# Performance work log

Hardware: AMD Instinct MI355X
Metric: run time of the kernel (lower is better)

## Reference

```python
import jax, jax.numpy as jnp
import numpy as np

B, C, H, W = 4, 512, 64, 64  # batch, channels (query_dim=model_dim), spatial

def _conv1x1(x, Wm, bias):
    # 1x1 conv == channel-mixing matmul: (b,c,h,w),(o,c) -> (b,o,h,w)
    return jnp.einsum('bchw,oc->bohw', x, Wm) + bias[None, :, None, None]

def setup_inputs() -> dict:
    key = jax.random.key(0)
    ks = jax.random.split(key, 9)
    s = 0.02
    return {
        'q':  jax.random.normal(ks[0], (B, C, H, W), dtype=jnp.float32),
        'Wq': jax.random.normal(ks[1], (C, C), dtype=jnp.float32) * s,
        'bq': jax.random.normal(ks[2], (C,), dtype=jnp.float32) * s,
        'Wk': jax.random.normal(ks[3], (C, C), dtype=jnp.float32) * s,
        'bk': jax.random.normal(ks[4], (C,), dtype=jnp.float32) * s,
        'Wv': jax.random.normal(ks[5], (C, C), dtype=jnp.float32) * s,
        'bv': jax.random.normal(ks[6], (C,), dtype=jnp.float32) * s,
        'Wo': jax.random.normal(ks[7], (C, C), dtype=jnp.float32) * s,
        'bo': jax.random.normal(ks[8], (C,), dtype=jnp.float32) * s,
    }

def reference(q, Wq, bq, Wk, bk, Wv, bv, Wo, bo):
    b, c, h, w = q.shape
    # separate=True, k=v=q (get_qkv defaults)
    qp = _conv1x1(q, Wq, bq)
    kp = _conv1x1(q, Wk, bk)
    vp = _conv1x1(q, Wv, bv)
    # view_in: b c h w -> b (h w) c  (single head; heads are NOT split)
    def flat(x):
        return x.reshape(b, c, h * w).transpose(0, 2, 1)  # (b, s, c)
    qf, kf, vf = flat(qp), flat(kp), flat(vp)
    scale = jnp.asarray(c, qf.dtype) ** -0.5  # q.shape[-1]^-0.5 = model_dim^-0.5
    sim = jnp.einsum('bqc,bkc->bqk', qf, kf) * scale  # (b, s, s)
    attn = jax.nn.softmax(sim, axis=-1)
    x = jnp.einsum('bqk,bkc->bqc', attn, vf)  # (b, s, c)
    x = x.transpose(0, 2, 1).reshape(b, c, h, w)  # view_out
    return _conv1x1(x, Wo, bo)
```

## Files before the change

kernel.cpp:

```cpp
#include <hip/hip_runtime.h>

typedef short bf16x8 __attribute__((ext_vector_type(8)));
typedef float f32x4 __attribute__((ext_vector_type(4)));
typedef long i64frag;

#define MFMA16(a, b, c) __builtin_amdgcn_mfma_f32_16x16x32_bf16((a), (b), (c), 0, 0, 0)
#define MFMA8(a, b, c) __builtin_amdgcn_mfma_f32_16x16x32_fp8_fp8((a), (b), (c), 0, 0, 0)

#define SEQ 4096
#define CD 512

#define LGKM0 asm volatile("s_waitcnt lgkmcnt(0)" ::: "memory")
#define VM0   asm volatile("s_waitcnt vmcnt(0)" ::: "memory")
#define VMC12 asm volatile("s_waitcnt vmcnt(12)" ::: "memory")

__device__ __forceinline__ unsigned short f2bf(float f) {
  unsigned u = __builtin_bit_cast(unsigned, f);
  u = u + 0x7FFFu + ((u >> 16) & 1u);
  return (unsigned short)(u >> 16);
}

__device__ __forceinline__ int pk4_fp8(float p0, float p1, float p2, float p3) {
  int w = __builtin_amdgcn_cvt_pk_fp8_f32(p0, p1, 0, false);
  w = __builtin_amdgcn_cvt_pk_fp8_f32(p2, p3, w, true);
  return w;
}

__device__ __forceinline__ void gload_lds16(const void* g, void* l) {
  __builtin_amdgcn_global_load_lds(
      (const __attribute__((address_space(1))) void*)g,
      (__attribute__((address_space(3))) void*)l, 16, 0, 0);
}

__global__ __launch_bounds__(256) void convert_w(
    const float* __restrict__ Wq, const float* __restrict__ Wk,
    const float* __restrict__ Wv, const float* __restrict__ Wo,
    const float* __restrict__ bq, const float* __restrict__ bk,
    const float* __restrict__ bv, const float* __restrict__ bo,
    unsigned short* __restrict__ W4, float* __restrict__ b4) {
  int i = blockIdx.x * 256 + threadIdx.x;
  int p = i >> 18, idx = i & 262143;
  const float sc = 1.4426950408889634f * 0.04419417382415922f;
  const float* W = (p == 0) ? Wq : (p == 1) ? Wk : (p == 2) ? Wv : Wo;
  float v = W[idx] * ((p == 0) ? sc : 1.0f);
  W4[i] = f2bf(v);
  if (idx < 512) {
    const float* bb = (p == 0) ? bq : (p == 1) ? bk : (p == 2) ? bv : bo;
    b4[(p << 9) + idx] = bb[idx] * ((p == 0) ? sc : 1.0f);
  }
}

__global__ __launch_bounds__(256) void transpose_q(
    const float* __restrict__ q, unsigned short* __restrict__ qT) {
  __shared__ float tile[64][65];
  const int b = blockIdx.z, c0 = blockIdx.y * 64, s0 = blockIdx.x * 64;
  const int t = threadIdx.x;
  const int lx = t & 15, ly = t >> 4;
  #pragma unroll
  for (int i = 0; i < 4; i++) {
    int c = ly + i * 16;
    f32x4 v = *(const f32x4*)&q[((size_t)b * CD + c0 + c) * SEQ + s0 + lx * 4];
    tile[c][lx * 4 + 0] = v[0];
    tile[c][lx * 4 + 1] = v[1];
    tile[c][lx * 4 + 2] = v[2];
    tile[c][lx * 4 + 3] = v[3];
  }
  __syncthreads();
  #pragma unroll
  for (int i = 0; i < 4; i++) {
    int s = ly + i * 16;
    ushort4 o;
    o.x = f2bf(tile[lx * 4 + 0][s]);
    o.y = f2bf(tile[lx * 4 + 1][s]);
    o.z = f2bf(tile[lx * 4 + 2][s]);
    o.w = f2bf(tile[lx * 4 + 3][s]);
    *(ushort4*)&qT[((size_t)b * SEQ + s0 + s) * CD + c0 + lx * 4] = o;
  }
}

__device__ __forceinline__ void gemm_core2(
    const unsigned short* __restrict__ Ap, size_t lda,
    const unsigned short* __restrict__ Bp, size_t ldb, int kmax,
    unsigned short* As, unsigned short* Bs, f32x4 acc[4][4]) {
  const int t = threadIdx.x;
  const int wid = t >> 6, lane = t & 63;
  const int l15 = lane & 15, l4 = lane >> 4;
  const int wr = wid >> 1, wc = wid & 1;
  for (int k0 = 0; k0 < kmax; k0 += 64) {
    #pragma unroll
    for (int j = 0; j < 4; j++) {
      int slot = j * 256 + t;
      int row = slot >> 3, kc = slot & 7;
      int kcs = kc ^ (row & 7);
      gload_lds16(Ap + (size_t)row * lda + k0 + kcs * 8, As + (j * 256 + wid * 64) * 8);
      gload_lds16(Bp + (size_t)row * ldb + k0 + kcs * 8, Bs + (j * 256 + wid * 64) * 8);
    }
    __syncthreads();
    #pragma unroll
    for (int ks = 0; ks < 2; ks++) {
      bf16x8 af[4], bf[4];
      #pragma unroll
      for (int i = 0; i < 4; i++) {
        int ra = wr * 64 + i * 16 + l15;
        af[i] = *(const bf16x8*)(As + ra * 64 + (((ks << 2) | l4) ^ (ra & 7)) * 8);
        int rb = wc * 64 + i * 16 + l15;
        bf[i] = *(const bf16x8*)(Bs + rb * 64 + (((ks << 2) | l4) ^ (rb & 7)) * 8);
      }
      #pragma unroll
      for (int i = 0; i < 4; i++)
        #pragma unroll
        for (int j = 0; j < 4; j++)
          acc[i][j] = MFMA16(af[i], bf[j], acc[i][j]);
    }
    __syncthreads();
  }
}

__device__ __forceinline__ void gemm_core(
    const unsigned short* __restrict__ Ap, const unsigned short* __restrict__ Bp,
    unsigned short* As, unsigned short* Bs, f32x4 acc[4][4]) {
  gemm_core2(Ap, 512, Bp, 512, 512, As, Bs, acc);
}

__global__ __launch_bounds__(512, 2) void gemm_proj256(
    const unsigned short* __restrict__ qT, const unsigned short* __restrict__ W4,
    const float* __restrict__ b4,
    unsigned short* __restrict__ Qf, unsigned short* __restrict__ Kf,
    unsigned short* __restrict__ VfT, unsigned char* __restrict__ Vf8) {
  __shared__ unsigned short As[2][2][128 * 64];
  __shared__ unsigned short Bs[2][2][128 * 64];

  const int tid = threadIdx.x;
  const int wid = tid >> 6, lane = tid & 63;
  const int l15 = lane & 15, l4 = lane >> 4;
  const int wm = wid >> 2, wn = wid & 3;

  const int id = blockIdx.x;
  const int xcd = id & 7;
  const int w = id >> 3;
  const int p = w >> 4;
  const int sub = w & 15;
  const int mt = (xcd << 3) | (sub >> 1);
  const int nt = sub & 1;
  const int m0 = mt * 256;
  const int n0 = nt * 256;

  const unsigned short* Ap = qT + (size_t)m0 * 512;
  const unsigned short* Bp = W4 + ((size_t)p * 512 + n0) * 512;

#define PJ_HALF(DST, SRC, HALF, K0)                                           \
  _Pragma("unroll")                                                           \
  for (int i_ = 0; i_ < 2; i_++) {                                            \
    int sg = i_ * 512 + tid;                                                  \
    int row = sg >> 3, kc = sg & 7;                                           \
    int kcs = kc ^ (row & 7);                                                 \
    gload_lds16(SRC + (size_t)((HALF) * 128 + row) * 512 + (K0) + kcs * 8,    \
                &DST[sg * 8]);                                                \
  }

  f32x4 acc[8][4];
  #pragma unroll
  for (int i = 0; i < 8; i++)
    #pragma unroll
    for (int j = 0; j < 4; j++) acc[i][j] = (f32x4){0.f, 0.f, 0.f, 0.f};

  PJ_HALF(As[0][0], Ap, 0, 0)
  PJ_HALF(As[0][1], Ap, 1, 0)
  PJ_HALF(Bs[0][0], Bp, 0, 0)
  PJ_HALF(Bs[0][1], Bp, 1, 0)
  VM0;
  __builtin_amdgcn_s_barrier();

  bf16x8 afr[4][2], bfr0[2][2], bfr1[2][2];
  const int bh = wn >> 1;
  const int brow = (wn & 1) * 64;

  for (int t = 0; t < 8; t++) {
    const int d = t & 1;
    const unsigned short* Ah = As[d][wm];
    const unsigned short* Bh = Bs[d][bh];
    const int k0n = (t + 1) * 64;
    const bool more = (t < 7);

    #pragma unroll
    for (int i = 0; i < 4; i++) {
      int r = i * 16 + l15;
      afr[i][0] = *(const bf16x8*)(Ah + r * 64 + ((l4) ^ (r & 7)) * 8);
      afr[i][1] = *(const bf16x8*)(Ah + r * 64 + ((4 | l4) ^ (r & 7)) * 8);
    }
    #pragma unroll
    for (int j = 0; j < 2; j++) {
      int r = brow + j * 16 + l15;
      bfr0[j][0] = *(const bf16x8*)(Bh + r * 64 + ((l4) ^ (r & 7)) * 8);
      bfr0[j][1] = *(const bf16x8*)(Bh + r * 64 + ((4 | l4) ^ (r & 7)) * 8);
    }
    if (more) {
      PJ_HALF(As[d ^ 1][0], Ap, 0, k0n)
      PJ_HALF(As[d ^ 1][1], Ap, 1, k0n)
    }
    __builtin_amdgcn_s_barrier();
    LGKM0;
    __builtin_amdgcn_s_setprio(1);
    #pragma unroll
    for (int ks = 0; ks < 2; ks++)
      #pragma unroll
      for (int i = 0; i < 4; i++)
        #pragma unroll
        for (int j = 0; j < 2; j++)
          acc[i][j] = MFMA16(afr[i][ks], bfr0[j][ks], acc[i][j]);
    __builtin_amdgcn_s_setprio(0);
    __builtin_amdgcn_s_barrier();

    #pragma unroll
    for (int j = 0; j < 2; j++) {
      int r = brow + (j + 2) * 16 + l15;
      bfr1[j][0] = *(const bf16x8*)(Bh + r * 64 + ((l4) ^ (r & 7)) * 8);
      bfr1[j][1] = *(const bf16x8*)(Bh + r * 64 + ((4 | l4) ^ (r & 7)) * 8);
    }
    if (more) {
      PJ_HALF(Bs[d ^ 1][0], Bp, 0, k0n)
      PJ_HALF(Bs[d ^ 1][1], Bp, 1, k0n)
    }
    __builtin_amdgcn_s_barrier();
    LGKM0;
    __builtin_amdgcn_s_setprio(1);
    #pragma unroll
    for (int ks = 0; ks < 2; ks++)
      #pragma unroll
      for (int i = 0; i < 4; i++)
        #pragma unroll
        for (int j = 0; j < 2; j++)
          acc[i][j + 2] = MFMA16(afr[i][ks], bfr1[j][ks], acc[i][j + 2]);
    __builtin_amdgcn_s_setprio(0);
    __builtin_amdgcn_s_barrier();

    #pragma unroll
    for (int i = 0; i < 4; i++) {
      int r = 64 + i * 16 + l15;
      afr[i][0] = *(const bf16x8*)(Ah + r * 64 + ((l4) ^ (r & 7)) * 8);
      afr[i][1] = *(const bf16x8*)(Ah + r * 64 + ((4 | l4) ^ (r & 7)) * 8);
    }
    __builtin_amdgcn_s_barrier();
    LGKM0;
    __builtin_amdgcn_s_setprio(1);
    #pragma unroll
    for (int ks = 0; ks < 2; ks++)
      #pragma unroll
      for (int i = 0; i < 4; i++)
        #pragma unroll
        for (int j = 0; j < 2; j++)
          acc[i + 4][j + 2] = MFMA16(afr[i][ks], bfr1[j][ks], acc[i + 4][j + 2]);
    __builtin_amdgcn_s_setprio(0);
    __builtin_amdgcn_s_barrier();

    __builtin_amdgcn_s_barrier();
    __builtin_amdgcn_s_setprio(1);
    #pragma unroll
    for (int ks = 0; ks < 2; ks++)
      #pragma unroll
      for (int i = 0; i < 4; i++)
        #pragma unroll
        for (int j = 0; j < 2; j++)
          acc[i + 4][j] = MFMA16(afr[i][ks], bfr0[j][ks], acc[i + 4][j]);
    __builtin_amdgcn_s_setprio(0);
    VM0;
    __builtin_amdgcn_s_barrier();
  }
#undef PJ_HALF

  if (p < 2) {
    unsigned short* out = (p == 0) ? Qf : Kf;
    #pragma unroll
    for (int i = 0; i < 8; i++) {
      int m = m0 + wm * 128 + i * 16 + l4 * 4;
      #pragma unroll
      for (int j = 0; j < 4; j++) {
        int n = n0 + wn * 64 + j * 16 + l15;
        float bias = b4[p * 512 + n];
        #pragma unroll
        for (int r = 0; r < 4; r++)
          out[(size_t)(m + r) * 512 + n] = f2bf(acc[i][j][r] + bias);
      }
    }
  } else {
    #pragma unroll
    for (int i = 0; i < 8; i++) {
      int m = m0 + wm * 128 + i * 16 + l4 * 4;
      int bb = m >> 12, sb = m & 4095;
      #pragma unroll
      for (int j = 0; j < 4; j++) {
        int n = n0 + wn * 64 + j * 16 + l15;
        float bias = b4[2 * 512 + n];
        float v0 = acc[i][j][0] + bias, v1 = acc[i][j][1] + bias;
        float v2 = acc[i][j][2] + bias, v3 = acc[i][j][3] + bias;
        if (VfT) {
          ushort4 v;
          v.x = f2bf(v0); v.y = f2bf(v1); v.z = f2bf(v2); v.w = f2bf(v3);
          *(ushort4*)&VfT[((size_t)bb * CD + n) * SEQ + sb] = v;
        }
        if (Vf8)
          *(int*)&Vf8[((size_t)bb * CD + n) * SEQ + sb] = pk4_fp8(v0, v1, v2, v3);
      }
    }
  }
}

__global__ __launch_bounds__(512, 2) void gemm_qk256(
    const unsigned short* __restrict__ Qf, const unsigned short* __restrict__ Kf,
    unsigned char* __restrict__ P8, float* __restrict__ partials,
    int bbase, int nbat) {
  __shared__ unsigned short As[2][2][128 * 64];
  __shared__ unsigned short Bs[2][2][128 * 64];
  __shared__ float ssum[2][4][4][16];

  const int tid = threadIdx.x;
  const int wid = tid >> 6, lane = tid & 63;
  const int l15 = lane & 15, l4 = lane >> 4;
  const int wm = wid >> 2, wn = wid & 3;

  const int id = blockIdx.x;
  const int xcd = id & 7;
  int z, qt, kt;
  if (nbat == 4) {
    z = xcd >> 1;
    int w = id >> 3;
    qt = ((xcd & 1) << 3) | (w >> 4);
    kt = w & 15;
  } else {
    z = 0;
    int w = id >> 3;
    qt = (xcd << 1) | (w >> 4);
    kt = w & 15;
  }
  const int b = bbase + z;
  const int m0 = kt * 256;
  const int n0 = qt * 256;

  const unsigned short* Ap = Kf + ((size_t)b * SEQ + m0) * CD;
  const unsigned short* Bp = Qf + ((size_t)b * SEQ + n0) * CD;

#define QK_HALF(DST, SRC, HALF, K0)                                           \
  _Pragma("unroll")                                                           \
  for (int i_ = 0; i_ < 2; i_++) {                                            \
    int sg = i_ * 512 + tid;                                                  \
    int row = sg >> 3, kc = sg & 7;                                           \
    int kcs = kc ^ (row & 7);                                                 \
    gload_lds16(SRC + (size_t)((HALF) * 128 + row) * CD + (K0) + kcs * 8,     \
                &DST[sg * 8]);                                                \
  }

  f32x4 acc[8][4];
  #pragma unroll
  for (int i = 0; i < 8; i++)
    #pragma unroll
    for (int j = 0; j < 4; j++) acc[i][j] = (f32x4){0.f, 0.f, 0.f, 0.f};

  QK_HALF(As[0][0], Ap, 0, 0)
  QK_HALF(As[0][1], Ap, 1, 0)
  QK_HALF(Bs[0][0], Bp, 0, 0)
  QK_HALF(Bs[0][1], Bp, 1, 0)
  VM0;
  __builtin_amdgcn_s_barrier();

  bf16x8 afr[4][2], bfr0[2][2], bfr1[2][2];
  const int bh = wn >> 1;
  const int brow = (wn & 1) * 64;

  for (int t = 0; t < 8; t++) {
    const int d = t & 1;
    const unsigned short* Ah = As[d][wm];
    const unsigned short* Bh = Bs[d][bh];
    const int k0n = (t + 1) * 64;
    const bool more = (t < 7);

    #pragma unroll
    for (int i = 0; i < 4; i++) {
      int r = i * 16 + l15;
      afr[i][0] = *(const bf16x8*)(Ah + r * 64 + ((l4) ^ (r & 7)) * 8);
      afr[i][1] = *(const bf16x8*)(Ah + r * 64 + ((4 | l4) ^ (r & 7)) * 8);
    }
    #pragma unroll
    for (int j = 0; j < 2; j++) {
      int r = brow + j * 16 + l15;
      bfr0[j][0] = *(const bf16x8*)(Bh + r * 64 + ((l4) ^ (r & 7)) * 8);
      bfr0[j][1] = *(const bf16x8*)(Bh + r * 64 + ((4 | l4) ^ (r & 7)) * 8);
    }
    if (more) {
      QK_HALF(As[d ^ 1][0], Ap, 0, k0n)
      QK_HALF(As[d ^ 1][1], Ap, 1, k0n)
    }
    __builtin_amdgcn_s_barrier();
    LGKM0;
    __builtin_amdgcn_s_setprio(1);
    #pragma unroll
    for (int ks = 0; ks < 2; ks++)
      #pragma unroll
      for (int i = 0; i < 4; i++)
        #pragma unroll
        for (int j = 0; j < 2; j++)
          acc[i][j] = MFMA16(afr[i][ks], bfr0[j][ks], acc[i][j]);
    __builtin_amdgcn_s_setprio(0);
    __builtin_amdgcn_s_barrier();

    #pragma unroll
    for (int j = 0; j < 2; j++) {
      int r = brow + (j + 2) * 16 + l15;
      bfr1[j][0] = *(const bf16x8*)(Bh + r * 64 + ((l4) ^ (r & 7)) * 8);
      bfr1[j][1] = *(const bf16x8*)(Bh + r * 64 + ((4 | l4) ^ (r & 7)) * 8);
    }
    if (more) {
      QK_HALF(Bs[d ^ 1][0], Bp, 0, k0n)
      QK_HALF(Bs[d ^ 1][1], Bp, 1, k0n)
    }
    __builtin_amdgcn_s_barrier();
    LGKM0;
    __builtin_amdgcn_s_setprio(1);
    #pragma unroll
    for (int ks = 0; ks < 2; ks++)
      #pragma unroll
      for (int i = 0; i < 4; i++)
        #pragma unroll
        for (int j = 0; j < 2; j++)
          acc[i][j + 2] = MFMA16(afr[i][ks], bfr1[j][ks], acc[i][j + 2]);
    __builtin_amdgcn_s_setprio(0);
    __builtin_amdgcn_s_barrier();

    #pragma unroll
    for (int i = 0; i < 4; i++) {
      int r = 64 + i * 16 + l15;
      afr[i][0] = *(const bf16x8*)(Ah + r * 64 + ((l4) ^ (r & 7)) * 8);
      afr[i][1] = *(const bf16x8*)(Ah + r * 64 + ((4 | l4) ^ (r & 7)) * 8);
    }
    __builtin_amdgcn_s_barrier();
    LGKM0;
    __builtin_amdgcn_s_setprio(1);
    #pragma unroll
    for (int ks = 0; ks < 2; ks++)
      #pragma unroll
      for (int i = 0; i < 4; i++)
        #pragma unroll
        for (int j = 0; j < 2; j++)
          acc[i + 4][j + 2] = MFMA16(afr[i][ks], bfr1[j][ks], acc[i + 4][j + 2]);
    __builtin_amdgcn_s_setprio(0);
    __builtin_amdgcn_s_barrier();

    __builtin_amdgcn_s_barrier();
    __builtin_amdgcn_s_setprio(1);
    #pragma unroll
    for (int ks = 0; ks < 2; ks++)
      #pragma unroll
      for (int i = 0; i < 4; i++)
        #pragma unroll
        for (int j = 0; j < 2; j++)
          acc[i + 4][j] = MFMA16(afr[i][ks], bfr0[j][ks], acc[i + 4][j]);
    __builtin_amdgcn_s_setprio(0);
    VM0;
    __builtin_amdgcn_s_barrier();
  }
#undef QK_HALF

  unsigned char* Pz = P8 + (size_t)z * SEQ * SEQ;
  float sj[4] = {0.f, 0.f, 0.f, 0.f};
  #pragma unroll
  for (int i = 0; i < 8; i++) {
    int m = m0 + wm * 128 + i * 16 + l4 * 4;
    #pragma unroll
    for (int j = 0; j < 4; j++) {
      int n = n0 + wn * 64 + j * 16 + l15;
      float p0 = __builtin_amdgcn_exp2f(acc[i][j][0]);
      float p1 = __builtin_amdgcn_exp2f(acc[i][j][1]);
      float p2 = __builtin_amdgcn_exp2f(acc[i][j][2]);
      float p3 = __builtin_amdgcn_exp2f(acc[i][j][3]);
      sj[j] += (p0 + p1) + (p2 + p3);
      *(int*)&Pz[(size_t)n * SEQ + m] = pk4_fp8(p0, p1, p2, p3);
    }
  }
  #pragma unroll
  for (int j = 0; j < 4; j++) {
    float s = sj[j];
    s += __shfl_xor(s, 16, 64);
    s += __shfl_xor(s, 32, 64);
    if (lane < 16) ssum[wm][wn][j][l15] = s;
  }
  __syncthreads();
  if (tid < 256) {
    int wn_ = tid >> 6, j_ = (tid >> 4) & 3, l_ = tid & 15;
    float s = ssum[0][wn_][j_][l_] + ssum[1][wn_][j_][l_];
    partials[((size_t)z * SEQ + n0 + tid) * 16 + kt] = s;
  }
}

__global__ __launch_bounds__(256) void reduce_l(
    const float* __restrict__ partials, float* __restrict__ linv) {
  int i = blockIdx.x * 256 + threadIdx.x;
  const float* p = partials + (size_t)i * 16;
  float s = 0.f;
  #pragma unroll
  for (int j = 0; j < 16; j++) s += p[j];
  linv[i] = 1.0f / s;
}

__global__ __launch_bounds__(256) void gemm_pv8(
    const unsigned char* __restrict__ Vf8, const unsigned char* __restrict__ P8,
    const float* __restrict__ linv, unsigned short* __restrict__ Ao,
    int bbase, int nbat) {
  __shared__ unsigned char As[128 * 128];
  __shared__ unsigned char Bs[64 * 128];
  const int tid = threadIdx.x;
  const int wid = tid >> 6, lane = tid & 63;
  const int l15 = lane & 15, l4 = lane >> 4;
  const int wr = wid >> 1, wc = wid & 1;

  const int id = blockIdx.x;
  const int xcd = id & 7;
  int z, qt, ct;
  if (nbat == 4) {
    z = xcd >> 1;
    int w = id >> 3;
    qt = ((xcd & 1) << 5) | (w >> 2);
    ct = w & 3;
  } else {
    z = 0;
    int w = id >> 3;
    qt = (xcd << 3) | (w >> 2);
    ct = w & 3;
  }
  const int b = bbase + z;
  const int n0 = qt * 64, m0 = ct * 128;

  const unsigned char* Ap = Vf8 + ((size_t)b * CD + m0) * SEQ;
  const unsigned char* Bp = P8 + (size_t)z * SEQ * SEQ + (size_t)n0 * SEQ;

  f32x4 acc[4][2];
  #pragma unroll
  for (int i = 0; i < 4; i++) {
    acc[i][0] = (f32x4){0.f, 0.f, 0.f, 0.f};
    acc[i][1] = (f32x4){0.f, 0.f, 0.f, 0.f};
  }

  for (int k0 = 0; k0 < SEQ; k0 += 128) {
    #pragma unroll
    for (int i = 0; i < 4; i++) {
      int sg = i * 256 + tid;
      int row = sg >> 3, kc = sg & 7;
      int kcs = kc ^ (row & 7);
      gload_lds16(Ap + (size_t)row * SEQ + k0 + kcs * 16, As + sg * 16);
    }
    #pragma unroll
    for (int i = 0; i < 2; i++) {
      int sg = i * 256 + tid;
      int row = sg >> 3, kc = sg & 7;
      int kcs = kc ^ (row & 7);
      gload_lds16(Bp + (size_t)row * SEQ + k0 + kcs * 16, Bs + sg * 16);
    }
    __syncthreads();
    #pragma unroll
    for (int ks = 0; ks < 4; ks++) {
      i64frag af[4], bf[2];
      const int ch = ks * 2 + (l4 >> 1);
      const int hb = (l4 & 1) * 8;
      #pragma unroll
      for (int i = 0; i < 4; i++) {
        int ra = wr * 64 + i * 16 + l15;
        af[i] = *(const i64frag*)(As + ra * 128 + (ch ^ (ra & 7)) * 16 + hb);
      }
      #pragma unroll
      for (int j = 0; j < 2; j++) {
        int rb = wc * 32 + j * 16 + l15;
        bf[j] = *(const i64frag*)(Bs + rb * 128 + (ch ^ (rb & 7)) * 16 + hb);
      }
      #pragma unroll
      for (int i = 0; i < 4; i++)
        #pragma unroll
        for (int j = 0; j < 2; j++)
          acc[i][j] = MFMA8(af[i], bf[j], acc[i][j]);
    }
    __syncthreads();
  }

  #pragma unroll
  for (int j = 0; j < 2; j++) {
    int n = n0 + wc * 32 + j * 16 + l15;
    float inv = linv[(size_t)z * SEQ + n];
    #pragma unroll
    for (int i = 0; i < 4; i++) {
      int m = m0 + wr * 64 + i * 16 + l4 * 4;
      ushort4 o4;
      o4.x = f2bf(acc[i][j][0] * inv);
      o4.y = f2bf(acc[i][j][1] * inv);
      o4.z = f2bf(acc[i][j][2] * inv);
      o4.w = f2bf(acc[i][j][3] * inv);
      *(ushort4*)&Ao[((size_t)b * SEQ + n) * CD + m] = o4;
    }
  }
}

#define SECTION(T, VRC, VRP, DOPV)                                              \
  {                                                                             \
    const int t_ = (T);                                                         \
    const unsigned short* vt_ = vbase + t_ * 32;                                \
    _Pragma("unroll")                                                           \
    for (int i = 0; i < 8; i++)                                                 \
      VRC[i] = *(const bf16x8*)(vt_ + (size_t)i * 16 * SEQ);                    \
    f32x4 sf = (f32x4){0.f, 0.f, 0.f, 0.f};                                     \
    __builtin_amdgcn_s_setprio(1);                                              \
    {                                                                           \
      const char* krow = (const char*)(Ks + (size_t)(t_ & 3) * 16384) +         \
                         (s * 16 + l15) * 1024;                                 \
      const int kswz = (l15 & 7) << 4;                                          \
      _Pragma("unroll")                                                         \
      for (int ck = 0; ck < 16; ck++) {                                         \
        bf16x8 kf = *(const bf16x8*)(krow + ((ck * 64 + l4 * 16) ^ kswz));      \
        sf = MFMA16(kf, qreg[ck], sf);                                          \
      }                                                                         \
    }                                                                           \
    if (DOPV) {                                                                 \
      _Pragma("unroll")                                                         \
      for (int jf = 0; jf < 2; jf++) {                                          \
        int qv = qw * 32 + jf * 16 + l15;                                       \
        bf16x8 pb = *(const bf16x8*)((const char*)Ps + ((t_ + 1) & 1) * 4096 +  \
                                     qv * 64 +                                  \
                                     ((l4 * 16) ^ (((qv >> 1) & 3) << 4)));     \
        _Pragma("unroll")                                                       \
        for (int i = 0; i < 8; i++)                                             \
          acc[i][jf] = MFMA16(VRP[i], pb, acc[i][jf]);                          \
      }                                                                         \
    }                                                                           \
    __builtin_amdgcn_s_setprio(0);                                              \
    {                                                                           \
      float p0 = __builtin_amdgcn_exp2f(sf[0]);                                 \
      float p1 = __builtin_amdgcn_exp2f(sf[1]);                                 \
      float p2 = __builtin_amdgcn_exp2f(sf[2]);                                 \
      float p3 = __builtin_amdgcn_exp2f(sf[3]);                                 \
      l_acc[0] += p0; l_acc[1] += p1; l_acc[2] += p2; l_acc[3] += p3;           \
      ushort4 pk;                                                               \
      pk.x = f2bf(p0); pk.y = f2bf(p1); pk.z = f2bf(p2); pk.w = f2bf(p3);       \
      int q_ = g * 16 + l15;                                                    \
      int off = (t_ & 1) * 4096 + q_ * 64 +                                     \
                ((s * 32 + l4 * 8) ^ (((q_ >> 1) & 3) << 4));                   \
      *(ushort4*)((char*)Ps + off) = pk;                                        \
    }                                                                           \
    {                                                                           \
      int tt = (t_ + 2 < 128) ? t_ + 2 : 127;                                   \
      const unsigned short* kn = kbT + (size_t)tt * 32 * CD;                    \
      unsigned short* kdst = Ks + (size_t)((t_ + 2) & 3) * 16384;               \
      _Pragma("unroll")                                                         \
      for (int i = 0; i < 4; i++) {                                             \
        int slot = i * 512 + tid;                                               \
        int row = slot >> 6, kc = slot & 63;                                    \
        int kcs = kc ^ (row & 7);                                               \
        gload_lds16(kn + (size_t)row * CD + kcs * 8,                            \
                    kdst + (size_t)(i * 512 + wid * 64) * 8);                   \
      }                                                                         \
    }                                                                           \
    LGKM0;                                                                      \
    VMC12;                                                                      \
    __builtin_amdgcn_s_barrier();                                               \
  }

__global__ __launch_bounds__(512, 2) void flash_attn(
    const unsigned short* __restrict__ Qf, const unsigned short* __restrict__ Kf,
    const unsigned short* __restrict__ VfT, unsigned short* __restrict__ Ao) {
  __shared__ unsigned short Ks[4 * 32 * 512];
  __shared__ unsigned short Ps[2 * 64 * 32];
  __shared__ float ssum[4][2][16];

  const int tid = threadIdx.x;
  const int wid = tid >> 6, lane = tid & 63;
  const int l15 = lane & 15, l4 = lane >> 4;
  const int s = wid & 1, g = wid >> 1;
  const int cw = wid & 3, qw = wid >> 2;

  const int id = blockIdx.x;
  const int xcd = id & 7;
  const int b = xcd >> 1;
  const int q0 = ((id >> 3) + ((xcd & 1) << 5)) * 64;

  const unsigned short* kbT = Kf + (size_t)b * SEQ * CD;
  const unsigned short* vbase = VfT + ((size_t)b * CD + cw * 128 + l15) * SEQ + l4 * 8;

  #pragma unroll
  for (int tt = 0; tt < 2; tt++) {
    const unsigned short* kn = kbT + (size_t)tt * 32 * CD;
    unsigned short* kdst = Ks + (size_t)tt * 16384;
    #pragma unroll
    for (int i = 0; i < 4; i++) {
      int slot = i * 512 + tid;
      int row = slot >> 6, kc = slot & 63;
      int kcs = kc ^ (row & 7);
      gload_lds16(kn + (size_t)row * CD + kcs * 8, kdst + (size_t)(i * 512 + wid * 64) * 8);
    }
  }

  bf16x8 qreg[16];
  {
    const unsigned short* qp = Qf + ((size_t)b * SEQ + q0 + g * 16 + l15) * CD + l4 * 8;
    #pragma unroll
    for (int ck = 0; ck < 16; ck++) qreg[ck] = *(const bf16x8*)(qp + ck * 32);
  }

  f32x4 acc[8][2];
  #pragma unroll
  for (int i = 0; i < 8; i++) {
    acc[i][0] = (f32x4){0.f, 0.f, 0.f, 0.f};
    acc[i][1] = (f32x4){0.f, 0.f, 0.f, 0.f};
  }
  f32x4 l_acc = (f32x4){0.f, 0.f, 0.f, 0.f};

  bf16x8 vrA[8], vrB[8];

  VM0;
  __builtin_amdgcn_s_barrier();

  SECTION(0, vrA, vrB, 0);
  for (int t = 1; t < 127; t += 2) {
    SECTION(t, vrB, vrA, 1);
    SECTION(t + 1, vrA, vrB, 1);
  }
  SECTION(127, vrB, vrA, 1);

  #pragma unroll
  for (int jf = 0; jf < 2; jf++) {
    int qv = qw * 32 + jf * 16 + l15;
    bf16x8 pb = *(const bf16x8*)((const char*)Ps + 4096 + qv * 64 +
                                 ((l4 * 16) ^ (((qv >> 1) & 3) << 4)));
    #pragma unroll
    for (int i = 0; i < 8; i++)
      acc[i][jf] = MFMA16(vrB[i], pb, acc[i][jf]);
  }

  float strip = (l_acc[0] + l_acc[1]) + (l_acc[2] + l_acc[3]);
  strip += __shfl_xor(strip, 16, 64);
  strip += __shfl_xor(strip, 32, 64);
  __syncthreads();
  if (lane < 16) ssum[g][s][l15] = strip;
  __syncthreads();

  #pragma unroll
  for (int jf = 0; jf < 2; jf++) {
    int gq = qw * 2 + jf;
    float inv = 1.0f / (ssum[gq][0][l15] + ssum[gq][1][l15]);
    #pragma unroll
    for (int i = 0; i < 8; i++) {
      int c0 = cw * 128 + i * 16 + l4 * 4;
      ushort4 o4;
      o4.x = f2bf(acc[i][jf][0] * inv);
      o4.y = f2bf(acc[i][jf][1] * inv);
      o4.z = f2bf(acc[i][jf][2] * inv);
      o4.w = f2bf(acc[i][jf][3] * inv);
      *(ushort4*)&Ao[((size_t)b * SEQ + q0 + qw * 32 + jf * 16 + l15) * CD + c0] = o4;
    }
  }
}

__global__ __launch_bounds__(256) void gemm_out(
    const unsigned short* __restrict__ W4, const float* __restrict__ b4,
    const unsigned short* __restrict__ Ao, float* __restrict__ out) {
  __shared__ unsigned short As[128 * 64], Bs[128 * 64];
  const int b = blockIdx.z;
  const int n0 = blockIdx.x * 128, m0 = blockIdx.y * 128;
  f32x4 acc[4][4];
  #pragma unroll
  for (int i = 0; i < 4; i++)
    #pragma unroll
    for (int j = 0; j < 4; j++) acc[i][j] = (f32x4){0.f, 0.f, 0.f, 0.f};
  gemm_core(W4 + ((size_t)3 * 512 + m0) * 512, Ao + ((size_t)b * SEQ + n0) * 512, As, Bs, acc);

  const int t = threadIdx.x;
  const int wid = t >> 6, lane = t & 63;
  const int l15 = lane & 15, l4 = lane >> 4;
  const int wr = wid >> 1, wc = wid & 1;
  #pragma unroll
  for (int i = 0; i < 4; i++) {
    int m = m0 + wr * 64 + i * 16 + l4 * 4;
    #pragma unroll
    for (int j = 0; j < 4; j++) {
      int n = n0 + wc * 64 + j * 16 + l15;
      #pragma unroll
      for (int r = 0; r < 4; r++)
        out[((size_t)b * CD + m + r) * SEQ + n] = acc[i][j][r] + b4[3 * 512 + m + r];
    }
  }
}

extern "C" void kernel_launch(void* const* d_in, const int* in_sizes, int n_in,
                              void* d_out, int out_size, void* d_ws, size_t ws_size,
                              hipStream_t stream) {
  (void)in_sizes; (void)n_in; (void)out_size;
  const float* q  = (const float*)d_in[0];
  const float* Wq = (const float*)d_in[1];
  const float* bq = (const float*)d_in[2];
  const float* Wk = (const float*)d_in[3];
  const float* bk = (const float*)d_in[4];
  const float* Wv = (const float*)d_in[5];
  const float* bv = (const float*)d_in[6];
  const float* Wo = (const float*)d_in[7];
  const float* bo = (const float*)d_in[8];
  float* out = (float*)d_out;

  char* ws = (char*)d_ws;
  const size_t MB = (size_t)1 << 20;
  unsigned short* qT  = (unsigned short*)(ws);
  unsigned short* Qf  = (unsigned short*)(ws + 16 * MB);
  unsigned short* Kf  = (unsigned short*)(ws + 32 * MB);
  unsigned short* VfT = (unsigned short*)(ws + 48 * MB);
  unsigned short* Ao = qT;

  if (ws_size >= 134 * MB) {
    unsigned char* P8    = (unsigned char*)(ws + 48 * MB);
    unsigned short* W4   = (unsigned short*)(ws + 112 * MB);
    float* b4            = (float*)(ws + 114 * MB);
    unsigned char* Vf8   = (unsigned char*)(ws + 115 * MB);
    float* partials      = (float*)(ws + 123 * MB);
    float* linv          = (float*)(ws + 124 * MB + 512 * 1024);

    convert_w<<<4096, 256, 0, stream>>>(Wq, Wk, Wv, Wo, bq, bk, bv, bo, W4, b4);
    transpose_q<<<dim3(64, 8, 4), 256, 0, stream>>>(q, qT);
    gemm_proj256<<<384, 512, 0, stream>>>(qT, W4, b4, Qf, Kf, (unsigned short*)nullptr, Vf8);
    gemm_qk256<<<1024, 512, 0, stream>>>(Qf, Kf, P8, partials, 0, 4);
    reduce_l<<<64, 256, 0, stream>>>(partials, linv);
    gemm_pv8<<<1024, 256, 0, stream>>>(Vf8, P8, linv, Ao, 0, 4);
    gemm_out<<<dim3(32, 4, 4), 256, 0, stream>>>(W4, b4, Ao, out);
  } else if (ws_size >= 101 * MB) {
    unsigned char* P8    = (unsigned char*)(ws + 48 * MB);
    unsigned short* W4   = (unsigned short*)(ws + 64 * MB);
    float* b4            = (float*)(ws + 66 * MB);
    unsigned char* Vf8   = (unsigned char*)(ws + 67 * MB);
    float* partials      = (float*)(ws + 75 * MB);
    float* linv          = (float*)(ws + 76 * MB);

    convert_w<<<4096, 256, 0, stream>>>(Wq, Wk, Wv, Wo, bq, bk, bv, bo, W4, b4);
    transpose_q<<<dim3(64, 8, 4), 256, 0, stream>>>(q, qT);
    gemm_proj256<<<384, 512, 0, stream>>>(qT, W4, b4, Qf, Kf, (unsigned short*)nullptr, Vf8);
    for (int bb = 0; bb < 4; ++bb) {
      gemm_qk256<<<256, 512, 0, stream>>>(Qf, Kf, P8, partials, bb, 1);
      reduce_l<<<16, 256, 0, stream>>>(partials, linv);
      gemm_pv8<<<256, 256, 0, stream>>>(Vf8, P8, linv, Ao, bb, 1);
    }
    gemm_out<<<dim3(32, 4, 4), 256, 0, stream>>>(W4, b4, Ao, out);
  } else {
    unsigned short* W4 = (unsigned short*)(ws + 64 * MB);
    float* b4          = (float*)(ws + 66 * MB);
    convert_w<<<4096, 256, 0, stream>>>(Wq, Wk, Wv, Wo, bq, bk, bv, bo, W4, b4);
    transpose_q<<<dim3(64, 8, 4), 256, 0, stream>>>(q, qT);
    gemm_proj256<<<384, 512, 0, stream>>>(qT, W4, b4, Qf, Kf, VfT, (unsigned char*)nullptr);
    flash_attn<<<256, 512, 0, stream>>>(Qf, Kf, VfT, Ao);
    gemm_out<<<dim3(32, 4, 4), 256, 0, stream>>>(W4, b4, Ao, out);
  }
}
```

Measured before the change: 230.2 us.

## Replace double-buffered QK tile pipeline with single-buffered load-sync-compute loop

```diff
diff --git a/kernel.cpp b/kernel.cpp
--- a/kernel.cpp
+++ b/kernel.cpp
@@ -309,8 +309,8 @@
     const unsigned short* __restrict__ Qf, const unsigned short* __restrict__ Kf,
     unsigned char* __restrict__ P8, float* __restrict__ partials,
     int bbase, int nbat) {
-  __shared__ unsigned short As[2][2][128 * 64];
-  __shared__ unsigned short Bs[2][2][128 * 64];
+  __shared__ unsigned short As[2][128 * 64];
+  __shared__ unsigned short Bs[2][128 * 64];
   __shared__ float ssum[2][4][4][16];
 
   const int tid = threadIdx.x;
@@ -355,23 +355,20 @@
     #pragma unroll
     for (int j = 0; j < 4; j++) acc[i][j] = (f32x4){0.f, 0.f, 0.f, 0.f};
 
-  QK_HALF(As[0][0], Ap, 0, 0)
-  QK_HALF(As[0][1], Ap, 1, 0)
-  QK_HALF(Bs[0][0], Bp, 0, 0)
-  QK_HALF(Bs[0][1], Bp, 1, 0)
-  VM0;
-  __builtin_amdgcn_s_barrier();
-
   bf16x8 afr[4][2], bfr0[2][2], bfr1[2][2];
   const int bh = wn >> 1;
   const int brow = (wn & 1) * 64;
 
   for (int t = 0; t < 8; t++) {
-    const int d = t & 1;
-    const unsigned short* Ah = As[d][wm];
-    const unsigned short* Bh = Bs[d][bh];
-    const int k0n = (t + 1) * 64;
-    const bool more = (t < 7);
+    const int k0 = t * 64;
+    QK_HALF(As[0], Ap, 0, k0)
+    QK_HALF(As[1], Ap, 1, k0)
+    QK_HALF(Bs[0], Bp, 0, k0)
+    QK_HALF(Bs[1], Bp, 1, k0)
+    __syncthreads();
+
+    const unsigned short* Ah = As[wm];
+    const unsigned short* Bh = Bs[bh];
 
     #pragma unroll
     for (int i = 0; i < 4; i++) {
@@ -385,12 +382,6 @@
       bfr0[j][0] = *(const bf16x8*)(Bh + r * 64 + ((l4) ^ (r & 7)) * 8);
       bfr0[j][1] = *(const bf16x8*)(Bh + r * 64 + ((4 | l4) ^ (r & 7)) * 8);
     }
-    if (more) {
-      QK_HALF(As[d ^ 1][0], Ap, 0, k0n)
-      QK_HALF(As[d ^ 1][1], Ap, 1, k0n)
-    }
-    __builtin_amdgcn_s_barrier();
-    LGKM0;
     __builtin_amdgcn_s_setprio(1);
     #pragma unroll
     for (int ks = 0; ks < 2; ks++)
@@ -400,7 +391,6 @@
         for (int j = 0; j < 2; j++)
           acc[i][j] = MFMA16(afr[i][ks], bfr0[j][ks], acc[i][j]);
     __builtin_amdgcn_s_setprio(0);
-    __builtin_amdgcn_s_barrier();
 
     #pragma unroll
     for (int j = 0; j < 2; j++) {
@@ -408,12 +398,6 @@
       bfr1[j][0] = *(const bf16x8*)(Bh + r * 64 + ((l4) ^ (r & 7)) * 8);
       bfr1[j][1] = *(const bf16x8*)(Bh + r * 64 + ((4 | l4) ^ (r & 7)) * 8);
     }
-    if (more) {
-      QK_HALF(Bs[d ^ 1][0], Bp, 0, k0n)
-      QK_HALF(Bs[d ^ 1][1], Bp, 1, k0n)
-    }
-    __builtin_amdgcn_s_barrier();
-    LGKM0;
     __builtin_amdgcn_s_setprio(1);
     #pragma unroll
     for (int ks = 0; ks < 2; ks++)
@@ -423,7 +407,6 @@
         for (int j = 0; j < 2; j++)
           acc[i][j + 2] = MFMA16(afr[i][ks], bfr1[j][ks], acc[i][j + 2]);
     __builtin_amdgcn_s_setprio(0);
-    __builtin_amdgcn_s_barrier();
 
     #pragma unroll
     for (int i = 0; i < 4; i++) {
@@ -431,8 +414,6 @@
       afr[i][0] = *(const bf16x8*)(Ah + r * 64 + ((l4) ^ (r & 7)) * 8);
       afr[i][1] = *(const bf16x8*)(Ah + r * 64 + ((4 | l4) ^ (r & 7)) * 8);
     }
-    __builtin_amdgcn_s_barrier();
-    LGKM0;
     __builtin_amdgcn_s_setprio(1);
     #pragma unroll
     for (int ks = 0; ks < 2; ks++)
@@ -441,11 +422,7 @@
         #pragma unroll
         for (int j = 0; j < 2; j++)
           acc[i + 4][j + 2] = MFMA16(afr[i][ks], bfr1[j][ks], acc[i + 4][j + 2]);
-    __builtin_amdgcn_s_setprio(0);
-    __builtin_amdgcn_s_barrier();
-
-    __builtin_amdgcn_s_barrier();
-    __builtin_amdgcn_s_setprio(1);
+
     #pragma unroll
     for (int ks = 0; ks < 2; ks++)
       #pragma unroll
@@ -454,8 +431,8 @@
         for (int j = 0; j < 2; j++)
           acc[i + 4][j] = MFMA16(afr[i][ks], bfr0[j][ks], acc[i + 4][j]);
     __builtin_amdgcn_s_setprio(0);
-    VM0;
-    __builtin_amdgcn_s_barrier();
+
+    __syncthreads();
   }
 #undef QK_HALF
 
```

Measured after the change: 234.5 us. No clear change (+1.8%).
